# Kernel tuning notes

Hardware: AMD Instinct MI355X
Metric: run time of the kernel (lower is better)

The kernel has to match this reference:

```python
import jax, jax.numpy as jnp
import numpy as np


def setup_inputs() -> dict:
    key = jax.random.key(0)
    ks = jax.random.split(key, 10)
    N, E = 50000, 1600000
    IN, H, OUT = 32, 64, 16
    x = jax.random.normal(ks[0], (N, IN), dtype=jnp.float32)
    edge_index = jax.random.randint(ks[1], (2, E), 0, N, dtype=jnp.int64)
    edge_attr = jax.random.normal(ks[2], (E, 3), dtype=jnp.float32)
    s1 = 1.0 / np.sqrt(2 * IN + 3)
    W1 = jax.random.uniform(ks[3], (2 * IN + 3, H), jnp.float32, -s1, s1)
    b1 = jax.random.uniform(ks[4], (H,), jnp.float32, -s1, s1)
    s2 = 1.0 / np.sqrt(H)
    W2 = jax.random.uniform(ks[5], (H, H), jnp.float32, -s2, s2)
    b2 = jax.random.uniform(ks[6], (H,), jnp.float32, -s2, s2)
    Wo = jax.random.uniform(ks[7], (H, OUT), jnp.float32, -s2, s2)
    bo = jax.random.uniform(ks[8], (OUT,), jnp.float32, -s2, s2)
    return {"x": x, "edge_index": edge_index, "edge_attr": edge_attr,
            "W1": W1, "b1": b1, "W2": W2, "b2": b2, "Wo": Wo, "bo": bo}


def reference(x, edge_index, edge_attr, W1, b1, W2, b2, Wo, bo):
    N = x.shape[0]
    src, dst = edge_index[0], edge_index[1]  # PyG: x_j = x[src], x_i = x[dst]
    x_i = x[dst]                      # [E, IN]
    x_j = x[src]                      # [E, IN]
    tmp = jnp.concatenate([x_i, x_j - x_i, edge_attr], axis=1)  # [E, 2*IN+3]
    h = jax.nn.relu(tmp @ W1 + b1)    # [E, H]
    msg = h @ W2 + b2                 # [E, H]
    # max-aggregate messages to destination nodes; empty segments -> 0 (PyG fill)
    agg = jax.ops.segment_max(msg, dst, num_segments=N)
    agg = jnp.where(jnp.isfinite(agg), agg, 0.0)
    out = jax.nn.sigmoid(agg @ Wo + bo)  # [N, OUT]
    return out
```

## Files before the change

### kernel.cpp

```cpp
#include <hip/hip_runtime.h>

#define IN_F 32
#define HID 64
#define OUTF 16
#define NSUB 8
#define SB_CAP 16
#define OVF_CAP 65536
#define ORD_NEG_INF 0x007FFFFFu

typedef _Float16 v8h __attribute__((ext_vector_type(8)));
typedef float v4f __attribute__((ext_vector_type(4)));

__device__ __forceinline__ unsigned ordenc(float v) {
  unsigned b = __float_as_uint(v);
  return (b & 0x80000000u) ? ~b : (b | 0x80000000u);
}
__device__ __forceinline__ float orddec(unsigned u) {
  unsigned b = (u & 0x80000000u) ? (u & 0x7FFFFFFFu) : ~u;
  return __uint_as_float(b);
}
__device__ __forceinline__ unsigned short f2h_bits(float f) {
  _Float16 h = (_Float16)f; unsigned short u; __builtin_memcpy(&u, &h, 2); return u;
}
__device__ __forceinline__ float h_bits2f(unsigned short u) {
  _Float16 h; __builtin_memcpy(&h, &u, 2); return (float)h;
}

__global__ __launch_bounds__(256) void pre_scatter_kernel(
    const float* __restrict__ x, const int* __restrict__ ei,
    const float* __restrict__ ea, const float* __restrict__ W1,
    const float* __restrict__ b1,
    float* __restrict__ P, float* __restrict__ Q,
    uint2* __restrict__ rec, int* __restrict__ cnt,
    int* __restrict__ ovf, int* __restrict__ ovf_cnt,
    int E, int N, int nSB)
{
  if (blockIdx.x < (unsigned)nSB) {
    const int t = threadIdx.x;
    const int base = blockIdx.x * 1024;
    const int g = blockIdx.x & (NSUB - 1);
    int e[4], s[4], d[4], pos[4];
    bool v[4];
#pragma unroll
    for (int i = 0; i < 4; ++i) {
      e[i] = base + i * 256 + t;
      v[i] = e[i] < E;
      int ec = v[i] ? e[i] : 0;
      s[i] = ei[ec];
      d[i] = ei[(size_t)E + ec];
    }
#pragma unroll
    for (int i = 0; i < 4; ++i)
      pos[i] = v[i] ? atomicAdd(&cnt[d[i] * NSUB + g], 1) : SB_CAP;
    float a0[4], a1[4], a2[4];
#pragma unroll
    for (int i = 0; i < 4; ++i) {
      int ec = v[i] ? e[i] : 0;
      a0[i] = ea[ec * 3 + 0]; a1[i] = ea[ec * 3 + 1]; a2[i] = ea[ec * 3 + 2];
    }
#pragma unroll
    for (int i = 0; i < 4; ++i) {
      if (!v[i]) continue;
      if (pos[i] < SB_CAP) {
        uint2 r;
        r.x = (unsigned)s[i] | ((unsigned)f2h_bits(a0[i]) << 16);
        r.y = (unsigned)f2h_bits(a1[i]) | ((unsigned)f2h_bits(a2[i]) << 16);
        rec[((size_t)d[i] * NSUB + g) * SB_CAP + pos[i]] = r;
      } else {
        int oi = atomicAdd(ovf_cnt, 1);
        if (oi < OVF_CAP) ovf[oi] = e[i];
      }
    }
    return;
  }
  const int lane = threadIdx.x & 63;
  float w1d[IN_F], w1b[IN_F];
#pragma unroll
  for (int c = 0; c < IN_F; ++c) {
    w1b[c] = W1[(IN_F + c) * HID + lane];
    w1d[c] = W1[c * HID + lane] - w1b[c];
  }
  const float b1v = b1[lane];
  int gw = __builtin_amdgcn_readfirstlane((((int)blockIdx.x - nSB) << 2) | (threadIdx.x >> 6));
  const int nwaves = 512 << 2;
  for (int n = gw; n < N; n += nwaves) {
    float p = b1v, q = 0.f;
#pragma unroll
    for (int c = 0; c < IN_F; ++c) {
      float xv = x[n * IN_F + c];
      p = fmaf(xv, w1d[c], p);
      q = fmaf(xv, w1b[c], q);
    }
    P[n * HID + lane] = p;
    Q[n * HID + lane] = q;
  }
}

__global__ __launch_bounds__(256) void bucket_kernel(
    const uint2* __restrict__ rec, const int* __restrict__ cnt,
    const float* __restrict__ W1, const float* __restrict__ W2,
    const float* __restrict__ P, const float* __restrict__ Q,
    unsigned* __restrict__ agg, int N)
{
  __shared__ __align__(16) _Float16 hB[4][16][72];
  __shared__ uint2 stage[4][2][NSUB * SB_CAP];

  const int wave = threadIdx.x >> 6;
  const int lane = threadIdx.x & 63;
  const int quad = lane >> 4;
  const int eidx = lane & 15;
  const int mych = ((eidx >> 2) << 4) + (quad << 2) + (eidx & 3);

  v8h a_frag[4][2];
#pragma unroll
  for (int t = 0; t < 4; ++t)
#pragma unroll
    for (int ks = 0; ks < 2; ++ks)
#pragma unroll
      for (int j = 0; j < 8; ++j)
        a_frag[t][ks][j] = (_Float16)W2[(ks * 32 + quad * 8 + j) * HID + t * 16 + eidx];

  const float w1c0 = W1[(2 * IN_F + 0) * HID + lane];
  const float w1c1 = W1[(2 * IN_F + 1) * HID + lane];
  const float w1c2 = W1[(2 * IN_F + 2) * HID + lane];

  const int gwave = __builtin_amdgcn_readfirstlane((blockIdx.x << 2) | wave);
  const int nw = gridDim.x << 2;

  int d = gwave;
  if (d >= N) return;

  int m; uint2 r0, r1; float pP;
  {
    const uint4 ca = *(const uint4*)&cnt[(size_t)d * NSUB];
    const uint4 cb = *(const uint4*)&cnt[(size_t)d * NSUB + 4];
    int c0 = min((int)ca.x, SB_CAP), c1 = min((int)ca.y, SB_CAP);
    int c2 = min((int)ca.z, SB_CAP), c3 = min((int)ca.w, SB_CAP);
    int c4 = min((int)cb.x, SB_CAP), c5 = min((int)cb.y, SB_CAP);
    int c6 = min((int)cb.z, SB_CAP), c7 = min((int)cb.w, SB_CAP);
    int p1 = c0, p2 = p1 + c1, p3 = p2 + c2, p4 = p3 + c3;
    int p5 = p4 + c4, p6 = p5 + c5, p7 = p6 + c6;
    m = p7 + c7;
#pragma unroll
    for (int rr = 0; rr < 2; ++rr) {
      int i = rr * 64 + lane;
      if (i < m) {
        int g = 0, base = 0;
        if (i >= p1) { g = 1; base = p1; }
        if (i >= p2) { g = 2; base = p2; }
        if (i >= p3) { g = 3; base = p3; }
        if (i >= p4) { g = 4; base = p4; }
        if (i >= p5) { g = 5; base = p5; }
        if (i >= p6) { g = 6; base = p6; }
        if (i >= p7) { g = 7; base = p7; }
        uint2 rv = rec[((size_t)d * NSUB + g) * SB_CAP + (i - base)];
        if (rr == 0) r0 = rv; else r1 = rv;
      }
    }
    pP = P[(size_t)d * HID + lane];
  }

  int cur = 0;
  while (d < N) {
    const int dn = d + nw;
    const int m_cur = m;
    const float pvl = pP;

    if (lane < m_cur) stage[wave][cur][lane] = r0;
    if (64 + lane < m_cur) stage[wave][cur][64 + lane] = r1;
    __builtin_amdgcn_wave_barrier();

    if (m_cur > 0) {
      float qv[16];
#pragma unroll
      for (int i = 0; i < 16; ++i) {
        int idx = min(i, m_cur - 1);
        uint2 rr = stage[wave][cur][idx];
        qv[i] = Q[(size_t)(rr.x & 0xFFFFu) * HID + lane];
      }

      if (dn < N) {
        const uint4 ca = *(const uint4*)&cnt[(size_t)dn * NSUB];
        const uint4 cb = *(const uint4*)&cnt[(size_t)dn * NSUB + 4];
        int c0 = min((int)ca.x, SB_CAP), c1 = min((int)ca.y, SB_CAP);
        int c2 = min((int)ca.z, SB_CAP), c3 = min((int)ca.w, SB_CAP);
        int c4 = min((int)cb.x, SB_CAP), c5 = min((int)cb.y, SB_CAP);
        int c6 = min((int)cb.z, SB_CAP), c7 = min((int)cb.w, SB_CAP);
        int p1 = c0, p2 = p1 + c1, p3 = p2 + c2, p4 = p3 + c3;
        int p5 = p4 + c4, p6 = p5 + c5, p7 = p6 + c6;
        m = p7 + c7;
#pragma unroll
        for (int rr = 0; rr < 2; ++rr) {
          int i = rr * 64 + lane;
          if (i < m) {
            int g = 0, base = 0;
            if (i >= p1) { g = 1; base = p1; }
            if (i >= p2) { g = 2; base = p2; }
            if (i >= p3) { g = 3; base = p3; }
            if (i >= p4) { g = 4; base = p4; }
            if (i >= p5) { g = 5; base = p5; }
            if (i >= p6) { g = 6; base = p6; }
            if (i >= p7) { g = 7; base = p7; }
            uint2 rv = rec[((size_t)dn * NSUB + g) * SB_CAP + (i - base)];
            if (rr == 0) r0 = rv; else r1 = rv;
          }
        }
        pP = P[(size_t)dn * HID + lane];
      }

      float maxv[4][4];
#pragma unroll
      for (int t = 0; t < 4; ++t)
#pragma unroll
        for (int r = 0; r < 4; ++r) maxv[t][r] = -INFINITY;

      const int ntile = (m_cur + 15) >> 4;
      for (int tb = 0; tb < ntile; ++tb) {
#pragma unroll
        for (int i = 0; i < 16; ++i) {
          int idx = min(tb * 16 + i, m_cur - 1);
          uint2 rr = stage[wave][cur][idx];
          float pre = pvl + qv[i];
          pre = fmaf(h_bits2f((unsigned short)(rr.x >> 16)), w1c0, pre);
          pre = fmaf(h_bits2f((unsigned short)(rr.y & 0xFFFFu)), w1c1, pre);
          pre = fmaf(h_bits2f((unsigned short)(rr.y >> 16)), w1c2, pre);
          hB[wave][i][lane] = (_Float16)fmaxf(pre, 0.f);
        }
        if (tb + 1 < ntile) {
#pragma unroll
          for (int i = 0; i < 16; ++i) {
            int idx = min((tb + 1) * 16 + i, m_cur - 1);
            uint2 rr = stage[wave][cur][idx];
            qv[i] = Q[(size_t)(rr.x & 0xFFFFu) * HID + lane];
          }
        }
        __builtin_amdgcn_wave_barrier();

        const v8h bf0 = *(const v8h*)&hB[wave][eidx][quad * 8];
        const v8h bf1 = *(const v8h*)&hB[wave][eidx][32 + quad * 8];
#pragma unroll
        for (int t = 0; t < 4; ++t) {
          v4f acc = (v4f){0.f, 0.f, 0.f, 0.f};
          acc = __builtin_amdgcn_mfma_f32_16x16x32_f16(a_frag[t][0], bf0, acc, 0, 0, 0);
          acc = __builtin_amdgcn_mfma_f32_16x16x32_f16(a_frag[t][1], bf1, acc, 0, 0, 0);
#pragma unroll
          for (int r = 0; r < 4; ++r) maxv[t][r] = fmaxf(maxv[t][r], acc[r]);
        }
        __builtin_amdgcn_wave_barrier();
      }

#pragma unroll
      for (int t = 0; t < 4; ++t)
#pragma unroll
        for (int r = 0; r < 4; ++r) {
          float v = maxv[t][r];
          v = fmaxf(v, __shfl_xor(v, 1, 64));
          v = fmaxf(v, __shfl_xor(v, 2, 64));
          v = fmaxf(v, __shfl_xor(v, 4, 64));
          v = fmaxf(v, __shfl_xor(v, 8, 64));
          maxv[t][r] = v;
        }
      float val = maxv[0][0];
#pragma unroll
      for (int t = 0; t < 4; ++t)
#pragma unroll
        for (int r = 0; r < 4; ++r)
          val = (eidx == t * 4 + r) ? maxv[t][r] : val;
      agg[(size_t)d * HID + mych] = ordenc(val);
    } else {
      if (dn < N) {
        const uint4 ca = *(const uint4*)&cnt[(size_t)dn * NSUB];
        const uint4 cb = *(const uint4*)&cnt[(size_t)dn * NSUB + 4];
        int c0 = min((int)ca.x, SB_CAP), c1 = min((int)ca.y, SB_CAP);
        int c2 = min((int)ca.z, SB_CAP), c3 = min((int)ca.w, SB_CAP);
        int c4 = min((int)cb.x, SB_CAP), c5 = min((int)cb.y, SB_CAP);
        int c6 = min((int)cb.z, SB_CAP), c7 = min((int)cb.w, SB_CAP);
        int p1 = c0, p2 = p1 + c1, p3 = p2 + c2, p4 = p3 + c3;
        int p5 = p4 + c4, p6 = p5 + c5, p7 = p6 + c6;
        m = p7 + c7;
#pragma unroll
        for (int rr = 0; rr < 2; ++rr) {
          int i = rr * 64 + lane;
          if (i < m) {
            int g = 0, base = 0;
            if (i >= p1) { g = 1; base = p1; }
            if (i >= p2) { g = 2; base = p2; }
            if (i >= p3) { g = 3; base = p3; }
            if (i >= p4) { g = 4; base = p4; }
            if (i >= p5) { g = 5; base = p5; }
            if (i >= p6) { g = 6; base = p6; }
            if (i >= p7) { g = 7; base = p7; }
            uint2 rv = rec[((size_t)dn * NSUB + g) * SB_CAP + (i - base)];
            if (rr == 0) r0 = rv; else r1 = rv;
          }
        }
        pP = P[(size_t)dn * HID + lane];
      }
      agg[(size_t)d * HID + lane] = ORD_NEG_INF;
    }
    d = dn; cur ^= 1;
  }
}

__global__ __launch_bounds__(256) void overflow_kernel(
    const int* __restrict__ ei, const float* __restrict__ ea,
    const float* __restrict__ W1, const float* __restrict__ W2,
    const float* __restrict__ P, const float* __restrict__ Q,
    const int* __restrict__ ovf, const int* __restrict__ ovf_cnt,
    unsigned* __restrict__ agg, int E)
{
  __shared__ float hsh[4][HID];
  const int wave = threadIdx.x >> 6;
  const int lane = threadIdx.x & 63;

  int M = *ovf_cnt;
  if (M > OVF_CAP) M = OVF_CAP;
  if (M == 0) return;

  float w2r[HID];
#pragma unroll
  for (int j = 0; j < HID; ++j) w2r[j] = W2[j * HID + lane];
  const float w1c0 = W1[(2 * IN_F + 0) * HID + lane];
  const float w1c1 = W1[(2 * IN_F + 1) * HID + lane];
  const float w1c2 = W1[(2 * IN_F + 2) * HID + lane];

  const int gwave = __builtin_amdgcn_readfirstlane((blockIdx.x << 2) | wave);
  const int nw = gridDim.x << 2;
  for (int k = gwave; k < M; k += nw) {
    int e = ovf[k];
    int s = ei[e];
    int d = ei[(size_t)E + e];
    float pre = P[(size_t)d * HID + lane] + Q[(size_t)s * HID + lane];
    pre = fmaf(ea[e * 3 + 0], w1c0, pre);
    pre = fmaf(ea[e * 3 + 1], w1c1, pre);
    pre = fmaf(ea[e * 3 + 2], w1c2, pre);
    hsh[wave][lane] = fmaxf(pre, 0.f);
    __builtin_amdgcn_wave_barrier();
    float mv = 0.f;
#pragma unroll
    for (int j = 0; j < HID; ++j) mv = fmaf(hsh[wave][j], w2r[j], mv);
    atomicMax(&agg[(size_t)d * HID + lane], ordenc(mv));
    __builtin_amdgcn_wave_barrier();
  }
}

__global__ __launch_bounds__(256) void out_kernel(
    const unsigned* __restrict__ agg,
    const float* __restrict__ b2,
    const float* __restrict__ Wo, const float* __restrict__ bo,
    float* __restrict__ out, int N)
{
  __shared__ float Wos[HID * OUTF];
  __shared__ float bos[OUTF];
  __shared__ float b2s[HID];
  __shared__ float aggs[16][HID + 1];

  for (int i = threadIdx.x; i < HID * OUTF; i += 256) Wos[i] = Wo[i];
  if (threadIdx.x < OUTF) bos[threadIdx.x] = bo[threadIdx.x];
  if (threadIdx.x < HID) b2s[threadIdx.x] = b2[threadIdx.x];
  __syncthreads();

  const int nodeBase = blockIdx.x * 16;
  {
    int ln = threadIdx.x >> 4;
    int k0 = (threadIdx.x & 15) * 4;
    int n = nodeBase + ln;
    if (n < N) {
      const uint4 u = *(const uint4*)&agg[n * HID + k0];
      aggs[ln][k0 + 0] = (u.x == ORD_NEG_INF) ? 0.f : orddec(u.x) + b2s[k0 + 0];
      aggs[ln][k0 + 1] = (u.y == ORD_NEG_INF) ? 0.f : orddec(u.y) + b2s[k0 + 1];
      aggs[ln][k0 + 2] = (u.z == ORD_NEG_INF) ? 0.f : orddec(u.z) + b2s[k0 + 2];
      aggs[ln][k0 + 3] = (u.w == ORD_NEG_INF) ? 0.f : orddec(u.w) + b2s[k0 + 3];
    }
  }
  __syncthreads();
  {
    int ln = threadIdx.x >> 4;
    int o = threadIdx.x & 15;
    int n = nodeBase + ln;
    if (n < N) {
      float acc = bos[o];
#pragma unroll
      for (int k = 0; k < HID; ++k) acc = fmaf(aggs[ln][k], Wos[k * OUTF + o], acc);
      out[n * OUTF + o] = 1.f / (1.f + __expf(-acc));
    }
  }
}

extern "C" void kernel_launch(void* const* d_in, const int* in_sizes, int n_in,
                              void* d_out, int out_size, void* d_ws, size_t ws_size,
                              hipStream_t stream) {
  const float* x  = (const float*)d_in[0];
  const int*   ei = (const int*)d_in[1];
  const float* ea = (const float*)d_in[2];
  const float* W1 = (const float*)d_in[3];
  const float* b1 = (const float*)d_in[4];
  const float* W2 = (const float*)d_in[5];
  const float* b2 = (const float*)d_in[6];
  const float* Wo = (const float*)d_in[7];
  const float* bo = (const float*)d_in[8];
  float* out = (float*)d_out;

  const int N = in_sizes[0] / IN_F;
  const int E = in_sizes[1] / 2;

  char* w = (char*)d_ws;
  float*    Pp  = (float*)w;                     w += (size_t)N * HID * 4;
  float*    Qp  = (float*)w;                     w += (size_t)N * HID * 4;
  unsigned* agg = (unsigned*)w;                  w += (size_t)N * HID * 4;
  uint2*    rec = (uint2*)w;                     w += (size_t)N * NSUB * SB_CAP * 8;
  int*      cnt = (int*)w;                       w += (size_t)N * NSUB * 4;
  int*  ovf_cnt = (int*)w;                       w += 16;
  int*      ovf = (int*)w;

  hipMemsetAsync(cnt, 0, (size_t)N * NSUB * 4 + 16, stream);

  const int nSB = (E + 1023) / 1024;
  pre_scatter_kernel<<<nSB + 512, 256, 0, stream>>>(
      x, ei, ea, W1, b1, Pp, Qp, rec, cnt, ovf, ovf_cnt, E, N, nSB);
  bucket_kernel<<<4096, 256, 0, stream>>>(rec, cnt, W1, W2, Pp, Qp, agg, N);
  overflow_kernel<<<256, 256, 0, stream>>>(ei, ea, W1, W2, Pp, Qp, ovf, ovf_cnt, agg, E);
  out_kernel<<<(N + 15) / 16, 256, 0, stream>>>(agg, b2, Wo, bo, out, N);
}
```

Measured before the change: 292.4 us.

## Bucket edges by XCC id with smaller per-bucket capacity and nontemporal loads

Uses the hardware XCC id as the sub-bucket index so counter atomics for a node stay within one XCC's L2. It moves the record layout to sub-bucket-major and halves per-bucket capacity, so each lane loads at most one record. It also doubles edges per scatter block and uses nontemporal loads for streamed inputs. The trade-off is that more edges may spill to the slower atomic overflow path, whose buffer is now bounded by E.

```diff
diff --git a/kernel.cpp b/kernel.cpp
--- a/kernel.cpp
+++ b/kernel.cpp
@@ -4,8 +4,7 @@
 #define HID 64
 #define OUTF 16
 #define NSUB 8
-#define SB_CAP 16
-#define OVF_CAP 65536
+#define SB_CAP 8
 #define ORD_NEG_INF 0x007FFFFFu
 
 typedef _Float16 v8h __attribute__((ext_vector_type(8)));
@@ -24,6 +23,12 @@
 }
 __device__ __forceinline__ float h_bits2f(unsigned short u) {
   _Float16 h; __builtin_memcpy(&h, &u, 2); return (float)h;
+}
+__device__ __forceinline__ int xcc_id() {
+  return (int)(__builtin_amdgcn_s_getreg(((4 - 1) << 11) | 20) & 7u);
+}
+__device__ __forceinline__ unsigned long long nt_load_u64(const unsigned long long* p) {
+  return __builtin_nontemporal_load(p);
 }
 
 __global__ __launch_bounds__(256) void pre_scatter_kernel(
@@ -31,44 +36,46 @@
     const float* __restrict__ ea, const float* __restrict__ W1,
     const float* __restrict__ b1,
     float* __restrict__ P, float* __restrict__ Q,
-    uint2* __restrict__ rec, int* __restrict__ cnt,
+    unsigned long long* __restrict__ rec, int* __restrict__ cnt,
     int* __restrict__ ovf, int* __restrict__ ovf_cnt,
     int E, int N, int nSB)
 {
   if (blockIdx.x < (unsigned)nSB) {
     const int t = threadIdx.x;
-    const int base = blockIdx.x * 1024;
-    const int g = blockIdx.x & (NSUB - 1);
-    int e[4], s[4], d[4], pos[4];
-    bool v[4];
-#pragma unroll
-    for (int i = 0; i < 4; ++i) {
+    const int base = blockIdx.x * 2048;
+    const int g = __builtin_amdgcn_readfirstlane(xcc_id());
+    int e[8], s[8], d[8], pos[8];
+    bool v[8];
+#pragma unroll
+    for (int i = 0; i < 8; ++i) {
       e[i] = base + i * 256 + t;
       v[i] = e[i] < E;
       int ec = v[i] ? e[i] : 0;
-      s[i] = ei[ec];
-      d[i] = ei[(size_t)E + ec];
-    }
-#pragma unroll
-    for (int i = 0; i < 4; ++i)
+      s[i] = __builtin_nontemporal_load(ei + ec);
+      d[i] = __builtin_nontemporal_load(ei + (size_t)E + ec);
+    }
+#pragma unroll
+    for (int i = 0; i < 8; ++i)
       pos[i] = v[i] ? atomicAdd(&cnt[d[i] * NSUB + g], 1) : SB_CAP;
-    float a0[4], a1[4], a2[4];
-#pragma unroll
-    for (int i = 0; i < 4; ++i) {
+    float a0[8], a1[8], a2[8];
+#pragma unroll
+    for (int i = 0; i < 8; ++i) {
       int ec = v[i] ? e[i] : 0;
-      a0[i] = ea[ec * 3 + 0]; a1[i] = ea[ec * 3 + 1]; a2[i] = ea[ec * 3 + 2];
-    }
-#pragma unroll
-    for (int i = 0; i < 4; ++i) {
+      a0[i] = __builtin_nontemporal_load(ea + ec * 3 + 0);
+      a1[i] = __builtin_nontemporal_load(ea + ec * 3 + 1);
+      a2[i] = __builtin_nontemporal_load(ea + ec * 3 + 2);
+    }
+#pragma unroll
+    for (int i = 0; i < 8; ++i) {
       if (!v[i]) continue;
       if (pos[i] < SB_CAP) {
-        uint2 r;
-        r.x = (unsigned)s[i] | ((unsigned)f2h_bits(a0[i]) << 16);
-        r.y = (unsigned)f2h_bits(a1[i]) | ((unsigned)f2h_bits(a2[i]) << 16);
-        rec[((size_t)d[i] * NSUB + g) * SB_CAP + pos[i]] = r;
+        unsigned lo = (unsigned)s[i] | ((unsigned)f2h_bits(a0[i]) << 16);
+        unsigned hi = (unsigned)f2h_bits(a1[i]) | ((unsigned)f2h_bits(a2[i]) << 16);
+        rec[((size_t)g * N + d[i]) * SB_CAP + pos[i]] =
+            (unsigned long long)lo | ((unsigned long long)hi << 32);
       } else {
         int oi = atomicAdd(ovf_cnt, 1);
-        if (oi < OVF_CAP) ovf[oi] = e[i];
+        if (oi < E) ovf[oi] = e[i];
       }
     }
     return;
@@ -97,13 +104,13 @@
 }
 
 __global__ __launch_bounds__(256) void bucket_kernel(
-    const uint2* __restrict__ rec, const int* __restrict__ cnt,
+    const unsigned long long* __restrict__ rec, const int* __restrict__ cnt,
     const float* __restrict__ W1, const float* __restrict__ W2,
     const float* __restrict__ P, const float* __restrict__ Q,
     unsigned* __restrict__ agg, int N)
 {
   __shared__ __align__(16) _Float16 hB[4][16][72];
-  __shared__ uint2 stage[4][2][NSUB * SB_CAP];
+  __shared__ unsigned long long stage[4][2][NSUB * SB_CAP];
 
   const int wave = threadIdx.x >> 6;
   const int lane = threadIdx.x & 63;
@@ -130,7 +137,7 @@
   int d = gwave;
   if (d >= N) return;
 
-  int m; uint2 r0, r1; float pP;
+  int m; unsigned long long r0 = 0; float pP;
   {
     const uint4 ca = *(const uint4*)&cnt[(size_t)d * NSUB];
     const uint4 cb = *(const uint4*)&cnt[(size_t)d * NSUB + 4];
@@ -141,21 +148,16 @@
     int p1 = c0, p2 = p1 + c1, p3 = p2 + c2, p4 = p3 + c3;
     int p5 = p4 + c4, p6 = p5 + c5, p7 = p6 + c6;
     m = p7 + c7;
-#pragma unroll
-    for (int rr = 0; rr < 2; ++rr) {
-      int i = rr * 64 + lane;
-      if (i < m) {
-        int g = 0, base = 0;
-        if (i >= p1) { g = 1; base = p1; }
-        if (i >= p2) { g = 2; base = p2; }
-        if (i >= p3) { g = 3; base = p3; }
-        if (i >= p4) { g = 4; base = p4; }
-        if (i >= p5) { g = 5; base = p5; }
-        if (i >= p6) { g = 6; base = p6; }
-        if (i >= p7) { g = 7; base = p7; }
-        uint2 rv = rec[((size_t)d * NSUB + g) * SB_CAP + (i - base)];
-        if (rr == 0) r0 = rv; else r1 = rv;
-      }
+    if (lane < m) {
+      int g = 0, base = 0;
+      if (lane >= p1) { g = 1; base = p1; }
+      if (lane >= p2) { g = 2; base = p2; }
+      if (lane >= p3) { g = 3; base = p3; }
+      if (lane >= p4) { g = 4; base = p4; }
+      if (lane >= p5) { g = 5; base = p5; }
+      if (lane >= p6) { g = 6; base = p6; }
+      if (lane >= p7) { g = 7; base = p7; }
+      r0 = nt_load_u64(&rec[((size_t)g * N + d) * SB_CAP + (lane - base)]);
     }
     pP = P[(size_t)d * HID + lane];
   }
@@ -167,7 +169,6 @@
     const float pvl = pP;
 
     if (lane < m_cur) stage[wave][cur][lane] = r0;
-    if (64 + lane < m_cur) stage[wave][cur][64 + lane] = r1;
     __builtin_amdgcn_wave_barrier();
 
     if (m_cur > 0) {
@@ -175,8 +176,8 @@
 #pragma unroll
       for (int i = 0; i < 16; ++i) {
         int idx = min(i, m_cur - 1);
-        uint2 rr = stage[wave][cur][idx];
-        qv[i] = Q[(size_t)(rr.x & 0xFFFFu) * HID + lane];
+        unsigned long long rr = stage[wave][cur][idx];
+        qv[i] = Q[(size_t)((unsigned)rr & 0xFFFFu) * HID + lane];
       }
 
       if (dn < N) {
@@ -189,21 +190,16 @@
         int p1 = c0, p2 = p1 + c1, p3 = p2 + c2, p4 = p3 + c3;
         int p5 = p4 + c4, p6 = p5 + c5, p7 = p6 + c6;
         m = p7 + c7;
-#pragma unroll
-        for (int rr = 0; rr < 2; ++rr) {
-          int i = rr * 64 + lane;
-          if (i < m) {
-            int g = 0, base = 0;
-            if (i >= p1) { g = 1; base = p1; }
-            if (i >= p2) { g = 2; base = p2; }
-            if (i >= p3) { g = 3; base = p3; }
-            if (i >= p4) { g = 4; base = p4; }
-            if (i >= p5) { g = 5; base = p5; }
-            if (i >= p6) { g = 6; base = p6; }
-            if (i >= p7) { g = 7; base = p7; }
-            uint2 rv = rec[((size_t)dn * NSUB + g) * SB_CAP + (i - base)];
-            if (rr == 0) r0 = rv; else r1 = rv;
-          }
+        if (lane < m) {
+          int g = 0, base = 0;
+          if (lane >= p1) { g = 1; base = p1; }
+          if (lane >= p2) { g = 2; base = p2; }
+          if (lane >= p3) { g = 3; base = p3; }
+          if (lane >= p4) { g = 4; base = p4; }
+          if (lane >= p5) { g = 5; base = p5; }
+          if (lane >= p6) { g = 6; base = p6; }
+          if (lane >= p7) { g = 7; base = p7; }
+          r0 = nt_load_u64(&rec[((size_t)g * N + dn) * SB_CAP + (lane - base)]);
         }
         pP = P[(size_t)dn * HID + lane];
       }
@@ -219,19 +215,19 @@
 #pragma unroll
         for (int i = 0; i < 16; ++i) {
           int idx = min(tb * 16 + i, m_cur - 1);
-          uint2 rr = stage[wave][cur][idx];
+          unsigned long long rr = stage[wave][cur][idx];
           float pre = pvl + qv[i];
-          pre = fmaf(h_bits2f((unsigned short)(rr.x >> 16)), w1c0, pre);
-          pre = fmaf(h_bits2f((unsigned short)(rr.y & 0xFFFFu)), w1c1, pre);
-          pre = fmaf(h_bits2f((unsigned short)(rr.y >> 16)), w1c2, pre);
+          pre = fmaf(h_bits2f((unsigned short)((unsigned)rr >> 16)), w1c0, pre);
+          pre = fmaf(h_bits2f((unsigned short)((unsigned)(rr >> 32) & 0xFFFFu)), w1c1, pre);
+          pre = fmaf(h_bits2f((unsigned short)(rr >> 48)), w1c2, pre);
           hB[wave][i][lane] = (_Float16)fmaxf(pre, 0.f);
         }
         if (tb + 1 < ntile) {
 #pragma unroll
           for (int i = 0; i < 16; ++i) {
             int idx = min((tb + 1) * 16 + i, m_cur - 1);
-            uint2 rr = stage[wave][cur][idx];
-            qv[i] = Q[(size_t)(rr.x & 0xFFFFu) * HID + lane];
+            unsigned long long rr = stage[wave][cur][idx];
+            qv[i] = Q[(size_t)((unsigned)rr & 0xFFFFu) * HID + lane];
           }
         }
         __builtin_amdgcn_wave_barrier();
@@ -278,21 +274,16 @@
         int p1 = c0, p2 = p1 + c1, p3 = p2 + c2, p4 = p3 + c3;
         int p5 = p4 + c4, p6 = p5 + c5, p7 = p6 + c6;
         m = p7 + c7;
-#pragma unroll
-        for (int rr = 0; rr < 2; ++rr) {
-          int i = rr * 64 + lane;
-          if (i < m) {
-            int g = 0, base = 0;
-            if (i >= p1) { g = 1; base = p1; }
-            if (i >= p2) { g = 2; base = p2; }
-            if (i >= p3) { g = 3; base = p3; }
-            if (i >= p4) { g = 4; base = p4; }
-            if (i >= p5) { g = 5; base = p5; }
-            if (i >= p6) { g = 6; base = p6; }
-            if (i >= p7) { g = 7; base = p7; }
-            uint2 rv = rec[((size_t)dn * NSUB + g) * SB_CAP + (i - base)];
-            if (rr == 0) r0 = rv; else r1 = rv;
-          }
+        if (lane < m) {
+          int g = 0, base = 0;
+          if (lane >= p1) { g = 1; base = p1; }
+          if (lane >= p2) { g = 2; base = p2; }
+          if (lane >= p3) { g = 3; base = p3; }
+          if (lane >= p4) { g = 4; base = p4; }
+          if (lane >= p5) { g = 5; base = p5; }
+          if (lane >= p6) { g = 6; base = p6; }
+          if (lane >= p7) { g = 7; base = p7; }
+          r0 = nt_load_u64(&rec[((size_t)g * N + dn) * SB_CAP + (lane - base)]);
         }
         pP = P[(size_t)dn * HID + lane];
       }
@@ -314,7 +305,7 @@
   const int lane = threadIdx.x & 63;
 
   int M = *ovf_cnt;
-  if (M > OVF_CAP) M = OVF_CAP;
+  if (M > E) M = E;
   if (M == 0) return;
 
   float w2r[HID];
@@ -324,7 +315,7 @@
   const float w1c1 = W1[(2 * IN_F + 1) * HID + lane];
   const float w1c2 = W1[(2 * IN_F + 2) * HID + lane];
 
-  const int gwave = __builtin_amdgcn_readfirstlane((blockIdx.x << 2) | wave);
+  const int gwave = __builtin_amdgcn_readfirstlane((blockIdx.x << 2) | (threadIdx.x >> 6));
   const int nw = gridDim.x << 2;
   for (int k = gwave; k < M; k += nw) {
     int e = ovf[k];
@@ -408,17 +399,17 @@
   float*    Pp  = (float*)w;                     w += (size_t)N * HID * 4;
   float*    Qp  = (float*)w;                     w += (size_t)N * HID * 4;
   unsigned* agg = (unsigned*)w;                  w += (size_t)N * HID * 4;
-  uint2*    rec = (uint2*)w;                     w += (size_t)N * NSUB * SB_CAP * 8;
+  unsigned long long* rec = (unsigned long long*)w;  w += (size_t)N * NSUB * SB_CAP * 8;
   int*      cnt = (int*)w;                       w += (size_t)N * NSUB * 4;
   int*  ovf_cnt = (int*)w;                       w += 16;
   int*      ovf = (int*)w;
 
-  hipMemsetAsync(cnt, 0, (size_t)N * NSUB * 4 + 16, stream);
-
-  const int nSB = (E + 1023) / 1024;
+  (void)hipMemsetAsync(cnt, 0, (size_t)N * NSUB * 4 + 16, stream);
+
+  const int nSB = (E + 2047) / 2048;
   pre_scatter_kernel<<<nSB + 512, 256, 0, stream>>>(
       x, ei, ea, W1, b1, Pp, Qp, rec, cnt, ovf, ovf_cnt, E, N, nSB);
   bucket_kernel<<<4096, 256, 0, stream>>>(rec, cnt, W1, W2, Pp, Qp, agg, N);
-  overflow_kernel<<<256, 256, 0, stream>>>(ei, ea, W1, W2, Pp, Qp, ovf, ovf_cnt, agg, E);
+  overflow_kernel<<<512, 256, 0, stream>>>(ei, ea, W1, W2, Pp, Qp, ovf, ovf_cnt, agg, E);
   out_kernel<<<(N + 15) / 16, 256, 0, stream>>>(agg, b2, Wo, bo, out, N);
 }
```

Measured after the change: 355.3 us. +21.5%, slower.

## Store Q table in fp16 and pre-decode edge records into shared float4 tiles

Applied to the files above, without the earlier changes.

The per-node Q projection is now stored as fp16, which halves the bytes of the random gather done for every edge in the bucket and overflow kernels. Edge records become 64-bit words, and each tile of 16 records is decoded once into a double-buffered shared float4 array. All lanes then read the decoded source index and edge attributes from there instead of every lane unpacking the halves itself. The cost is lower precision in the Q term, plus extra LDS traffic and wave barriers.

```diff
diff --git a/kernel.cpp b/kernel.cpp
--- a/kernel.cpp
+++ b/kernel.cpp
@@ -30,8 +30,8 @@
     const float* __restrict__ x, const int* __restrict__ ei,
     const float* __restrict__ ea, const float* __restrict__ W1,
     const float* __restrict__ b1,
-    float* __restrict__ P, float* __restrict__ Q,
-    uint2* __restrict__ rec, int* __restrict__ cnt,
+    float* __restrict__ P, _Float16* __restrict__ Qh,
+    unsigned long long* __restrict__ rec, int* __restrict__ cnt,
     int* __restrict__ ovf, int* __restrict__ ovf_cnt,
     int E, int N, int nSB)
 {
@@ -62,10 +62,10 @@
     for (int i = 0; i < 4; ++i) {
       if (!v[i]) continue;
       if (pos[i] < SB_CAP) {
-        uint2 r;
-        r.x = (unsigned)s[i] | ((unsigned)f2h_bits(a0[i]) << 16);
-        r.y = (unsigned)f2h_bits(a1[i]) | ((unsigned)f2h_bits(a2[i]) << 16);
-        rec[((size_t)d[i] * NSUB + g) * SB_CAP + pos[i]] = r;
+        unsigned lo = (unsigned)s[i] | ((unsigned)f2h_bits(a0[i]) << 16);
+        unsigned hi = (unsigned)f2h_bits(a1[i]) | ((unsigned)f2h_bits(a2[i]) << 16);
+        rec[((size_t)d[i] * NSUB + g) * SB_CAP + pos[i]] =
+            (unsigned long long)lo | ((unsigned long long)hi << 32);
       } else {
         int oi = atomicAdd(ovf_cnt, 1);
         if (oi < OVF_CAP) ovf[oi] = e[i];
@@ -92,18 +92,19 @@
       q = fmaf(xv, w1b[c], q);
     }
     P[n * HID + lane] = p;
-    Q[n * HID + lane] = q;
+    Qh[n * HID + lane] = (_Float16)q;
   }
 }
 
 __global__ __launch_bounds__(256) void bucket_kernel(
-    const uint2* __restrict__ rec, const int* __restrict__ cnt,
+    const unsigned long long* __restrict__ rec, const int* __restrict__ cnt,
     const float* __restrict__ W1, const float* __restrict__ W2,
-    const float* __restrict__ P, const float* __restrict__ Q,
+    const float* __restrict__ P, const _Float16* __restrict__ Qh,
     unsigned* __restrict__ agg, int N)
 {
   __shared__ __align__(16) _Float16 hB[4][16][72];
-  __shared__ uint2 stage[4][2][NSUB * SB_CAP];
+  __shared__ unsigned long long stage[4][2][NSUB * SB_CAP];
+  __shared__ __align__(16) float4 eaT[4][2][16];
 
   const int wave = threadIdx.x >> 6;
   const int lane = threadIdx.x & 63;
@@ -130,7 +131,7 @@
   int d = gwave;
   if (d >= N) return;
 
-  int m; uint2 r0, r1; float pP;
+  int m; unsigned long long r0 = 0, r1 = 0; float pP;
   {
     const uint4 ca = *(const uint4*)&cnt[(size_t)d * NSUB];
     const uint4 cb = *(const uint4*)&cnt[(size_t)d * NSUB + 4];
@@ -153,7 +154,7 @@
         if (i >= p5) { g = 5; base = p5; }
         if (i >= p6) { g = 6; base = p6; }
         if (i >= p7) { g = 7; base = p7; }
-        uint2 rv = rec[((size_t)d * NSUB + g) * SB_CAP + (i - base)];
+        unsigned long long rv = rec[((size_t)d * NSUB + g) * SB_CAP + (i - base)];
         if (rr == 0) r0 = rv; else r1 = rv;
       }
     }
@@ -171,12 +172,25 @@
     __builtin_amdgcn_wave_barrier();
 
     if (m_cur > 0) {
+      const int ntile = (m_cur + 15) >> 4;
+
+      if (lane < 16) {
+        int idx = min(lane, m_cur - 1);
+        unsigned long long rr = stage[wave][cur][idx];
+        unsigned lo = (unsigned)rr, hi = (unsigned)(rr >> 32);
+        eaT[wave][0][lane] = make_float4(
+            __uint_as_float(lo & 0xFFFFu),
+            h_bits2f((unsigned short)(lo >> 16)),
+            h_bits2f((unsigned short)(hi & 0xFFFFu)),
+            h_bits2f((unsigned short)(hi >> 16)));
+      }
+      __builtin_amdgcn_wave_barrier();
+
       float qv[16];
 #pragma unroll
       for (int i = 0; i < 16; ++i) {
-        int idx = min(i, m_cur - 1);
-        uint2 rr = stage[wave][cur][idx];
-        qv[i] = Q[(size_t)(rr.x & 0xFFFFu) * HID + lane];
+        unsigned s = __float_as_uint(eaT[wave][0][i].x);
+        qv[i] = (float)Qh[(size_t)s * HID + lane];
       }
 
       if (dn < N) {
@@ -201,7 +215,7 @@
             if (i >= p5) { g = 5; base = p5; }
             if (i >= p6) { g = 6; base = p6; }
             if (i >= p7) { g = 7; base = p7; }
-            uint2 rv = rec[((size_t)dn * NSUB + g) * SB_CAP + (i - base)];
+            unsigned long long rv = rec[((size_t)dn * NSUB + g) * SB_CAP + (i - base)];
             if (rr == 0) r0 = rv; else r1 = rv;
           }
         }
@@ -214,24 +228,33 @@
 #pragma unroll
         for (int r = 0; r < 4; ++r) maxv[t][r] = -INFINITY;
 
-      const int ntile = (m_cur + 15) >> 4;
       for (int tb = 0; tb < ntile; ++tb) {
+        const int nbuf = (tb + 1) & 1;
+        if (tb + 1 < ntile && lane < 16) {
+          int idx = min((tb + 1) * 16 + lane, m_cur - 1);
+          unsigned long long rr = stage[wave][cur][idx];
+          unsigned lo = (unsigned)rr, hi = (unsigned)(rr >> 32);
+          eaT[wave][nbuf][lane] = make_float4(
+              __uint_as_float(lo & 0xFFFFu),
+              h_bits2f((unsigned short)(lo >> 16)),
+              h_bits2f((unsigned short)(hi & 0xFFFFu)),
+              h_bits2f((unsigned short)(hi >> 16)));
+        }
 #pragma unroll
         for (int i = 0; i < 16; ++i) {
-          int idx = min(tb * 16 + i, m_cur - 1);
-          uint2 rr = stage[wave][cur][idx];
+          const float4 tt = eaT[wave][tb & 1][i];
           float pre = pvl + qv[i];
-          pre = fmaf(h_bits2f((unsigned short)(rr.x >> 16)), w1c0, pre);
-          pre = fmaf(h_bits2f((unsigned short)(rr.y & 0xFFFFu)), w1c1, pre);
-          pre = fmaf(h_bits2f((unsigned short)(rr.y >> 16)), w1c2, pre);
+          pre = fmaf(tt.y, w1c0, pre);
+          pre = fmaf(tt.z, w1c1, pre);
+          pre = fmaf(tt.w, w1c2, pre);
           hB[wave][i][lane] = (_Float16)fmaxf(pre, 0.f);
         }
         if (tb + 1 < ntile) {
+          __builtin_amdgcn_wave_barrier();
 #pragma unroll
           for (int i = 0; i < 16; ++i) {
-            int idx = min((tb + 1) * 16 + i, m_cur - 1);
-            uint2 rr = stage[wave][cur][idx];
-            qv[i] = Q[(size_t)(rr.x & 0xFFFFu) * HID + lane];
+            unsigned s = __float_as_uint(eaT[wave][nbuf][i].x);
+            qv[i] = (float)Qh[(size_t)s * HID + lane];
           }
         }
         __builtin_amdgcn_wave_barrier();
@@ -290,7 +313,7 @@
             if (i >= p5) { g = 5; base = p5; }
             if (i >= p6) { g = 6; base = p6; }
             if (i >= p7) { g = 7; base = p7; }
-            uint2 rv = rec[((size_t)dn * NSUB + g) * SB_CAP + (i - base)];
+            unsigned long long rv = rec[((size_t)dn * NSUB + g) * SB_CAP + (i - base)];
             if (rr == 0) r0 = rv; else r1 = rv;
           }
         }
@@ -305,7 +328,7 @@
 __global__ __launch_bounds__(256) void overflow_kernel(
     const int* __restrict__ ei, const float* __restrict__ ea,
     const float* __restrict__ W1, const float* __restrict__ W2,
-    const float* __restrict__ P, const float* __restrict__ Q,
+    const float* __restrict__ P, const _Float16* __restrict__ Qh,
     const int* __restrict__ ovf, const int* __restrict__ ovf_cnt,
     unsigned* __restrict__ agg, int E)
 {
@@ -330,7 +353,7 @@
     int e = ovf[k];
     int s = ei[e];
     int d = ei[(size_t)E + e];
-    float pre = P[(size_t)d * HID + lane] + Q[(size_t)s * HID + lane];
+    float pre = P[(size_t)d * HID + lane] + (float)Qh[(size_t)s * HID + lane];
     pre = fmaf(ea[e * 3 + 0], w1c0, pre);
     pre = fmaf(ea[e * 3 + 1], w1c1, pre);
     pre = fmaf(ea[e * 3 + 2], w1c2, pre);
@@ -405,20 +428,20 @@
   const int E = in_sizes[1] / 2;
 
   char* w = (char*)d_ws;
-  float*    Pp  = (float*)w;                     w += (size_t)N * HID * 4;
-  float*    Qp  = (float*)w;                     w += (size_t)N * HID * 4;
+  float*     Pp = (float*)w;                     w += (size_t)N * HID * 4;
+  _Float16*  Qh = (_Float16*)w;                  w += (size_t)N * HID * 2;
   unsigned* agg = (unsigned*)w;                  w += (size_t)N * HID * 4;
-  uint2*    rec = (uint2*)w;                     w += (size_t)N * NSUB * SB_CAP * 8;
+  unsigned long long* rec = (unsigned long long*)w;  w += (size_t)N * NSUB * SB_CAP * 8;
   int*      cnt = (int*)w;                       w += (size_t)N * NSUB * 4;
   int*  ovf_cnt = (int*)w;                       w += 16;
   int*      ovf = (int*)w;
 
-  hipMemsetAsync(cnt, 0, (size_t)N * NSUB * 4 + 16, stream);
+  (void)hipMemsetAsync(cnt, 0, (size_t)N * NSUB * 4 + 16, stream);
 
   const int nSB = (E + 1023) / 1024;
   pre_scatter_kernel<<<nSB + 512, 256, 0, stream>>>(
-      x, ei, ea, W1, b1, Pp, Qp, rec, cnt, ovf, ovf_cnt, E, N, nSB);
-  bucket_kernel<<<4096, 256, 0, stream>>>(rec, cnt, W1, W2, Pp, Qp, agg, N);
-  overflow_kernel<<<256, 256, 0, stream>>>(ei, ea, W1, W2, Pp, Qp, ovf, ovf_cnt, agg, E);
+      x, ei, ea, W1, b1, Pp, Qh, rec, cnt, ovf, ovf_cnt, E, N, nSB);
+  bucket_kernel<<<4096, 256, 0, stream>>>(rec, cnt, W1, W2, Pp, Qh, agg, N);
+  overflow_kernel<<<256, 256, 0, stream>>>(ei, ea, W1, W2, Pp, Qh, ovf, ovf_cnt, agg, E);
   out_kernel<<<(N + 15) / 16, 256, 0, stream>>>(agg, b2, Wo, bo, out, N);
 }
```

Result: slower. 304.3 us (+4.0%).
